# Optimization experiments

Hardware: AMD Instinct MI355X
Metric: run time of the kernel (lower is better)

The kernel has to match this reference:

```python
import jax, jax.numpy as jnp
import numpy as np

N_NODES = 100000
N_EDGES = 640000
D_IN = 128
D_OUT = 128


def setup_inputs() -> dict:
    key = jax.random.key(0)
    k_x, k_w, k_v, k_r, k_c = jax.random.split(key, 5)
    x = jax.random.normal(k_x, (N_NODES, D_IN), dtype=jnp.float32)
    # Xavier-uniform init for weights, zeros for bias (matches module init)
    limit = float(np.sqrt(6.0 / (D_IN + D_OUT)))
    weights = jax.random.uniform(k_w, (D_IN, D_OUT), dtype=jnp.float32,
                                 minval=-limit, maxval=limit)
    bias = jnp.zeros((D_OUT,), dtype=jnp.float32)
    # Sparse normalized adjacency in COO form: value[e] * y[col[e]] scattered to row[e]
    edge_val = jax.random.uniform(k_v, (N_EDGES,), dtype=jnp.float32)
    row = jax.random.randint(k_r, (N_EDGES,), 0, N_NODES, dtype=jnp.int32)
    col = jax.random.randint(k_c, (N_EDGES,), 0, N_NODES, dtype=jnp.int32)
    return {"x": x, "weights": weights, "bias": bias,
            "edge_val": edge_val, "row": row, "col": col}


def reference(x, weights, bias, edge_val, row, col):
    # y = x @ W  (dense GEMM)  [N, D_OUT]
    y = x @ weights
    # SpMM: out[i] = sum_{e: row[e]==i} edge_val[e] * y[col[e]]
    msg = edge_val[:, None] * y[col]            # [E, D_OUT] irregular gather
    agg = jax.ops.segment_sum(msg, row, num_segments=x.shape[0])
    return agg + bias
```

## Files before the change

### kernel.cpp

```cpp
#include <hip/hip_runtime.h>
#include <hip/hip_bf16.h>


#define N_NODES 100000
#define N_EDGES 640000
#define D 128
#define ELL_K 16
#define OVF_CAP 8192
#define NB 391
#define BCAP 2048
#define CHUNK 4096
#define NCHUNKS 157
#define GEMM_BLOCKS 782
#define N_TILES 6250

typedef __attribute__((ext_vector_type(8))) short short8;
typedef __attribute__((ext_vector_type(4))) float f32x4;
typedef __attribute__((ext_vector_type(4))) ushort us4;

__device__ __forceinline__ ushort f2bf(float f) {
    uint u = __float_as_uint(f);
    u += 0x7fff + ((u >> 16) & 1);
    return (ushort)(u >> 16);
}
__device__ __forceinline__ float bflo(uint u) { return __uint_as_float(u << 16); }
__device__ __forceinline__ float bfhi(uint u) { return __uint_as_float(u & 0xffff0000u); }

__global__ __launch_bounds__(256, 2) void gemm_partition(const float* __restrict__ x,
                                                         const float* __restrict__ w,
                                                         ushort* __restrict__ y,
                                                         const float* __restrict__ ev,
                                                         const int* __restrict__ row,
                                                         const int* __restrict__ col,
                                                         int* __restrict__ bucketCnt,
                                                         uint2* __restrict__ es0,
                                                         int* __restrict__ ovfCnt,
                                                         int* __restrict__ ovfRow,
                                                         int* __restrict__ ovfCol,
                                                         float* __restrict__ ovfVal) {
    __shared__ union {
        ushort wt[128 * 128];
        struct { int hist[NB]; int cur[NB]; } p;
    } sm;
    const int tid = threadIdx.x;

    if (blockIdx.x < NCHUNKS) {
        const int base = blockIdx.x * CHUNK;
        for (int t = tid; t < NB; t += 256) sm.p.hist[t] = 0;
        __syncthreads();

        #pragma unroll
        for (int it = 0; it < CHUNK / 256; ++it) {
            int i = base + it * 256 + tid;
            if (i < N_EDGES) atomicAdd(&sm.p.hist[row[i] >> 8], 1);
        }
        __syncthreads();

        for (int t = tid; t < NB; t += 256) {
            int h = sm.p.hist[t];
            int start = (h > 0) ? atomicAdd(&bucketCnt[t], h) : 0;
            sm.p.cur[t] = t * BCAP + start;
        }
        __syncthreads();

        #pragma unroll
        for (int it = 0; it < CHUNK / 256; ++it) {
            int i = base + it * 256 + tid;
            if (i < N_EDGES) {
                int r = row[i];
                int b = r >> 8;
                int p = atomicAdd(&sm.p.cur[b], 1);
                if (p < (b + 1) * BCAP) {
                    uint2 e;
                    e.x = __float_as_uint(ev[i]);
                    e.y = (uint)col[i] | ((uint)(r & 255) << 20);
                    es0[p] = e;
                } else {
                    int q = atomicAdd(ovfCnt, 1);
                    if (q < OVF_CAP) {
                        ovfRow[q] = r;
                        ovfCol[q] = col[i];
                        ovfVal[q] = ev[i];
                    }
                }
            }
        }
        return;
    }

    const int bid = blockIdx.x - NCHUNKS;

    #pragma unroll
    for (int it = 0; it < 16; ++it) {
        int idx4 = tid + it * 256;
        int k = idx4 >> 5;
        int n0 = (idx4 & 31) * 4;
        float4 v = *(const float4*)(w + (size_t)idx4 * 4);
        float vv[4] = {v.x, v.y, v.z, v.w};
        #pragma unroll
        for (int q = 0; q < 4; ++q) {
            int n = n0 + q;
            sm.wt[n * 128 + (k ^ ((n & 7) << 3))] = f2bf(vv[q]);
        }
    }
    __syncthreads();

    const int lane = tid & 63;
    const int l15 = lane & 15;
    const int h = lane >> 4;

    short8 bfr[8][4];
    #pragma unroll
    for (int j = 0; j < 8; ++j) {
        int n = 16 * j + l15;
        #pragma unroll
        for (int ks = 0; ks < 4; ++ks) {
            int k0 = 32 * ks + 8 * h;
            bfr[j][ks] = *(const short8*)&sm.wt[n * 128 + (k0 ^ ((n & 7) << 3))];
        }
    }

    const int t0 = bid * 8 + (tid >> 6) * 2;
    #pragma unroll 1
    for (int rep = 0; rep < 2; ++rep) {
        int t = t0 + rep;
        if (t >= N_TILES) continue;
        const float* xr = x + (size_t)(t * 16 + l15) * D;
        float4 xb[8];
        #pragma unroll
        for (int ks = 0; ks < 4; ++ks) {
            xb[2 * ks]     = *(const float4*)(xr + 32 * ks + 8 * h);
            xb[2 * ks + 1] = *(const float4*)(xr + 32 * ks + 8 * h + 4);
        }
        f32x4 acc[8];
        #pragma unroll
        for (int j = 0; j < 8; ++j) acc[j] = (f32x4){0.f, 0.f, 0.f, 0.f};
        #pragma unroll
        for (int ks = 0; ks < 4; ++ks) {
            const float* p0 = (const float*)&xb[2 * ks];
            const float* p1 = (const float*)&xb[2 * ks + 1];
            short8 a;
            a[0] = f2bf(p0[0]); a[1] = f2bf(p0[1]); a[2] = f2bf(p0[2]); a[3] = f2bf(p0[3]);
            a[4] = f2bf(p1[0]); a[5] = f2bf(p1[1]); a[6] = f2bf(p1[2]); a[7] = f2bf(p1[3]);
            #pragma unroll
            for (int j = 0; j < 8; ++j)
                acc[j] = __builtin_amdgcn_mfma_f32_16x16x32_bf16(bfr[j][ks], a, acc[j], 0, 0, 0);
        }
        ushort* yn = y + (size_t)(t * 16 + l15) * D;
        #pragma unroll
        for (int j = 0; j < 8; ++j) {
            us4 o;
            o.x = f2bf(acc[j][0]); o.y = f2bf(acc[j][1]);
            o.z = f2bf(acc[j][2]); o.w = f2bf(acc[j][3]);
            *(us4*)(yn + 16 * j + 4 * h) = o;
        }
    }
}

__global__ __launch_bounds__(256) void build_ell(const uint2* __restrict__ es0,
                                                 const int* __restrict__ bucketCnt,
                                                 float2* __restrict__ es,
                                                 int* __restrict__ counts,
                                                 int* __restrict__ ovfCnt,
                                                 int* __restrict__ ovfRow,
                                                 int* __restrict__ ovfCol,
                                                 float* __restrict__ ovfVal) {
    __shared__ float2 ell[256 * ELL_K];
    __shared__ int lcnt[256];
    const int tid = threadIdx.x;
    const int b = blockIdx.x;

    lcnt[tid] = 0;
    __syncthreads();

    int cnt = bucketCnt[b];
    if (cnt > BCAP) cnt = BCAP;
    const uint2* src = es0 + (size_t)b * BCAP;

    for (int i = tid; i < cnt; i += 256) {
        uint2 e = src[i];
        int r = e.y >> 20;
        int p = atomicAdd(&lcnt[r], 1);
        if (p < ELL_K) {
            float2 rec;
            rec.x = __uint_as_float(e.x);
            rec.y = __uint_as_float(e.y & 0xFFFFFu);
            ell[r * ELL_K + p] = rec;
        } else {
            int q = atomicAdd(ovfCnt, 1);
            if (q < OVF_CAP) {
                ovfRow[q] = b * 256 + r;
                ovfCol[q] = (int)(e.y & 0xFFFFFu);
                ovfVal[q] = __uint_as_float(e.x);
            }
        }
    }
    __syncthreads();

    const int nbase = b * 256;
    int nvalid = N_NODES - nbase;
    if (nvalid > 256) nvalid = 256;

    if (tid < nvalid) counts[nbase + tid] = lcnt[tid];

    float4* dst4 = (float4*)(es + (size_t)nbase * ELL_K);
    const float4* ell4 = (const float4*)ell;
    for (int t = tid; t < nvalid * (ELL_K / 2); t += 256)
        dst4[t] = ell4[t];
}

__global__ __launch_bounds__(256) void spmm_ell(const ushort* __restrict__ y,
                                                const float2* __restrict__ es,
                                                const int* __restrict__ counts,
                                                const float* __restrict__ bias,
                                                float* __restrict__ out) {
    const int tid = threadIdx.x;
    const int lane = tid & 63;
    const int c16 = lane & 15;
    const int sub = lane >> 4;
    const int wid = blockIdx.x * 4 + (tid >> 6);

    const float4 b0 = *(const float4*)(bias + c16 * 8);
    const float4 b1 = *(const float4*)(bias + c16 * 8 + 4);

    #pragma unroll 1
    for (int rep = 0; rep < 2; ++rep) {
        const int n = wid * 8 + rep * 4 + sub;
        int deg = counts[n];
        if (deg > ELL_K) deg = ELL_K;
        const float4* er = (const float4*)(es + (size_t)n * ELL_K);

        float a0 = 0.f, a1 = 0.f, a2 = 0.f, a3 = 0.f;
        float a4 = 0.f, a5 = 0.f, a6 = 0.f, a7 = 0.f;

        #pragma unroll
        for (int g = 0; g < 4; ++g) {
            if (4 * g < deg) {
                float4 sA = er[2 * g];
                float4 sB = er[2 * g + 1];
                int c0 = __float_as_int(sA.y);
                int c1 = (4 * g + 1 < deg) ? __float_as_int(sA.w) : c0;
                int c2 = (4 * g + 2 < deg) ? __float_as_int(sB.y) : c0;
                int c3 = (4 * g + 3 < deg) ? __float_as_int(sB.w) : c0;
                uint4 u0 = *(const uint4*)(y + ((size_t)c0 << 7) + c16 * 8);
                uint4 u1 = *(const uint4*)(y + ((size_t)c1 << 7) + c16 * 8);
                uint4 u2 = *(const uint4*)(y + ((size_t)c2 << 7) + c16 * 8);
                uint4 u3 = *(const uint4*)(y + ((size_t)c3 << 7) + c16 * 8);
                float v0 = sA.x;
                float v1 = (4 * g + 1 < deg) ? sA.z : 0.f;
                float v2 = (4 * g + 2 < deg) ? sB.x : 0.f;
                float v3 = (4 * g + 3 < deg) ? sB.z : 0.f;
                a0 += v0 * bflo(u0.x); a1 += v0 * bfhi(u0.x);
                a2 += v0 * bflo(u0.y); a3 += v0 * bfhi(u0.y);
                a4 += v0 * bflo(u0.z); a5 += v0 * bfhi(u0.z);
                a6 += v0 * bflo(u0.w); a7 += v0 * bfhi(u0.w);
                a0 += v1 * bflo(u1.x); a1 += v1 * bfhi(u1.x);
                a2 += v1 * bflo(u1.y); a3 += v1 * bfhi(u1.y);
                a4 += v1 * bflo(u1.z); a5 += v1 * bfhi(u1.z);
                a6 += v1 * bflo(u1.w); a7 += v1 * bfhi(u1.w);
                a0 += v2 * bflo(u2.x); a1 += v2 * bfhi(u2.x);
                a2 += v2 * bflo(u2.y); a3 += v2 * bfhi(u2.y);
                a4 += v2 * bflo(u2.z); a5 += v2 * bfhi(u2.z);
                a6 += v2 * bflo(u2.w); a7 += v2 * bfhi(u2.w);
                a0 += v3 * bflo(u3.x); a1 += v3 * bfhi(u3.x);
                a2 += v3 * bflo(u3.y); a3 += v3 * bfhi(u3.y);
                a4 += v3 * bflo(u3.z); a5 += v3 * bfhi(u3.z);
                a6 += v3 * bflo(u3.w); a7 += v3 * bfhi(u3.w);
            }
        }
        float4 o0 = {a0 + b0.x, a1 + b0.y, a2 + b0.z, a3 + b0.w};
        float4 o1 = {a4 + b1.x, a5 + b1.y, a6 + b1.z, a7 + b1.w};
        float* orow = out + ((size_t)n << 7) + c16 * 8;
        *(float4*)orow = o0;
        *(float4*)(orow + 4) = o1;
    }
}

__global__ void ovf_fix(const ushort* __restrict__ y, const int* __restrict__ ovfRow,
                        const int* __restrict__ ovfCol, const float* __restrict__ ovfVal,
                        const int* __restrict__ ovfCnt, float* __restrict__ out) {
    int nOvf = *ovfCnt;
    if (nOvf > OVF_CAP) nOvf = OVF_CAP;
    int total = nOvf * 32;
    for (int idx = blockIdx.x * 256 + threadIdx.x; idx < total; idx += gridDim.x * 256) {
        int e = idx >> 5;
        int c = idx & 31;
        int r = ovfRow[e];
        int col = ovfCol[e];
        float v = ovfVal[e];
        uint2 u = *(const uint2*)(y + ((size_t)col << 7) + c * 4);
        atomicAdd(&out[(size_t)r * D + c * 4 + 0], v * bflo(u.x));
        atomicAdd(&out[(size_t)r * D + c * 4 + 1], v * bfhi(u.x));
        atomicAdd(&out[(size_t)r * D + c * 4 + 2], v * bflo(u.y));
        atomicAdd(&out[(size_t)r * D + c * 4 + 3], v * bfhi(u.y));
    }
}

extern "C" void kernel_launch(void* const* d_in, const int* in_sizes, int n_in,
                              void* d_out, int out_size, void* d_ws, size_t ws_size,
                              hipStream_t stream) {
    const float* x = (const float*)d_in[0];
    const float* w = (const float*)d_in[1];
    const float* bias = (const float*)d_in[2];
    const float* ev = (const float*)d_in[3];
    const int* row = (const int*)d_in[4];
    const int* col = (const int*)d_in[5];
    float* out = (float*)d_out;

    size_t off = 0;
    auto carve = [&](size_t bytes) -> void* {
        void* p = (char*)d_ws + off;
        off += (bytes + 255) & ~(size_t)255;
        return p;
    };
    ushort* y = (ushort*)carve((size_t)N_NODES * D * sizeof(ushort));
    int* counts = (int*)carve((size_t)N_NODES * sizeof(int));
    float2* es = (float2*)carve((size_t)N_NODES * ELL_K * sizeof(float2));
    uint2* es0 = (uint2*)carve((size_t)NB * BCAP * sizeof(uint2));
    int* bucketCnt = (int*)carve((NB + 1) * sizeof(int));
    int* ovfCnt = bucketCnt + NB;
    int* ovfRow = (int*)carve(OVF_CAP * sizeof(int));
    int* ovfCol = (int*)carve(OVF_CAP * sizeof(int));
    float* ovfVal = (float*)carve(OVF_CAP * sizeof(float));

    hipMemsetAsync(bucketCnt, 0, (NB + 1) * sizeof(int), stream);

    gemm_partition<<<NCHUNKS + GEMM_BLOCKS, 256, 0, stream>>>(
        x, w, y, ev, row, col, bucketCnt, es0, ovfCnt, ovfRow, ovfCol, ovfVal);
    build_ell<<<NB, 256, 0, stream>>>(es0, bucketCnt, es, counts,
                                      ovfCnt, ovfRow, ovfCol, ovfVal);
    spmm_ell<<<N_NODES / 32, 256, 0, stream>>>(y, es, counts, bias, out);
    ovf_fix<<<16, 256, 0, stream>>>(y, ovfRow, ovfCol, ovfVal, ovfCnt, out);
}
```

Measured before the change: 86.94 us.

## Split fused GEMM/partition kernel and software-pipeline persistent GEMM waves

Splits the combined GEMM-plus-edge-partition kernel into a persistent GEMM kernel with a grid-stride tile loop that prefetches the next x tile while the current tile's MFMAs run, followed by a separate partition kernel. The bucket counter reset moves from a memset into the GEMM kernel, which removes one launch. The cost is that partitioning no longer runs concurrently with the GEMM, and there is an extra kernel boundary.

```diff
diff --git a/kernel.cpp b/kernel.cpp
--- a/kernel.cpp
+++ b/kernel.cpp
@@ -11,7 +11,6 @@
 #define BCAP 2048
 #define CHUNK 4096
 #define NCHUNKS 157
-#define GEMM_BLOCKS 782
 #define N_TILES 6250
 
 typedef __attribute__((ext_vector_type(8))) short short8;
@@ -26,69 +25,15 @@
 __device__ __forceinline__ float bflo(uint u) { return __uint_as_float(u << 16); }
 __device__ __forceinline__ float bfhi(uint u) { return __uint_as_float(u & 0xffff0000u); }
 
-__global__ __launch_bounds__(256, 2) void gemm_partition(const float* __restrict__ x,
-                                                         const float* __restrict__ w,
-                                                         ushort* __restrict__ y,
-                                                         const float* __restrict__ ev,
-                                                         const int* __restrict__ row,
-                                                         const int* __restrict__ col,
-                                                         int* __restrict__ bucketCnt,
-                                                         uint2* __restrict__ es0,
-                                                         int* __restrict__ ovfCnt,
-                                                         int* __restrict__ ovfRow,
-                                                         int* __restrict__ ovfCol,
-                                                         float* __restrict__ ovfVal) {
-    __shared__ union {
-        ushort wt[128 * 128];
-        struct { int hist[NB]; int cur[NB]; } p;
-    } sm;
+__global__ __launch_bounds__(256, 2) void gemm_xw(const float* __restrict__ x,
+                                                  const float* __restrict__ w,
+                                                  ushort* __restrict__ y,
+                                                  int* __restrict__ bucketCnt) {
+    __shared__ ushort wt[128 * 128];
     const int tid = threadIdx.x;
 
-    if (blockIdx.x < NCHUNKS) {
-        const int base = blockIdx.x * CHUNK;
-        for (int t = tid; t < NB; t += 256) sm.p.hist[t] = 0;
-        __syncthreads();
-
-        #pragma unroll
-        for (int it = 0; it < CHUNK / 256; ++it) {
-            int i = base + it * 256 + tid;
-            if (i < N_EDGES) atomicAdd(&sm.p.hist[row[i] >> 8], 1);
-        }
-        __syncthreads();
-
-        for (int t = tid; t < NB; t += 256) {
-            int h = sm.p.hist[t];
-            int start = (h > 0) ? atomicAdd(&bucketCnt[t], h) : 0;
-            sm.p.cur[t] = t * BCAP + start;
-        }
-        __syncthreads();
-
-        #pragma unroll
-        for (int it = 0; it < CHUNK / 256; ++it) {
-            int i = base + it * 256 + tid;
-            if (i < N_EDGES) {
-                int r = row[i];
-                int b = r >> 8;
-                int p = atomicAdd(&sm.p.cur[b], 1);
-                if (p < (b + 1) * BCAP) {
-                    uint2 e;
-                    e.x = __float_as_uint(ev[i]);
-                    e.y = (uint)col[i] | ((uint)(r & 255) << 20);
-                    es0[p] = e;
-                } else {
-                    int q = atomicAdd(ovfCnt, 1);
-                    if (q < OVF_CAP) {
-                        ovfRow[q] = r;
-                        ovfCol[q] = col[i];
-                        ovfVal[q] = ev[i];
-                    }
-                }
-            }
-        }
-        return;
-    }
-
-    const int bid = blockIdx.x - NCHUNKS;
+    int gz = blockIdx.x * 256 + tid;
+    if (gz <= NB) bucketCnt[gz] = 0;
 
     #pragma unroll
     for (int it = 0; it < 16; ++it) {
@@ -100,7 +45,7 @@
         #pragma unroll
         for (int q = 0; q < 4; ++q) {
             int n = n0 + q;
-            sm.wt[n * 128 + (k ^ ((n & 7) << 3))] = f2bf(vv[q]);
+            wt[n * 128 + (k ^ ((n & 7) << 3))] = f2bf(vv[q]);
         }
     }
     __syncthreads();
@@ -116,43 +61,133 @@
         #pragma unroll
         for (int ks = 0; ks < 4; ++ks) {
             int k0 = 32 * ks + 8 * h;
-            bfr[j][ks] = *(const short8*)&sm.wt[n * 128 + (k0 ^ ((n & 7) << 3))];
-        }
-    }
-
-    const int t0 = bid * 8 + (tid >> 6) * 2;
-    #pragma unroll 1
-    for (int rep = 0; rep < 2; ++rep) {
-        int t = t0 + rep;
-        if (t >= N_TILES) continue;
-        const float* xr = x + (size_t)(t * 16 + l15) * D;
-        float4 xb[8];
-        #pragma unroll
-        for (int ks = 0; ks < 4; ++ks) {
-            xb[2 * ks]     = *(const float4*)(xr + 32 * ks + 8 * h);
-            xb[2 * ks + 1] = *(const float4*)(xr + 32 * ks + 8 * h + 4);
-        }
-        f32x4 acc[8];
-        #pragma unroll
-        for (int j = 0; j < 8; ++j) acc[j] = (f32x4){0.f, 0.f, 0.f, 0.f};
-        #pragma unroll
-        for (int ks = 0; ks < 4; ++ks) {
-            const float* p0 = (const float*)&xb[2 * ks];
-            const float* p1 = (const float*)&xb[2 * ks + 1];
-            short8 a;
-            a[0] = f2bf(p0[0]); a[1] = f2bf(p0[1]); a[2] = f2bf(p0[2]); a[3] = f2bf(p0[3]);
-            a[4] = f2bf(p1[0]); a[5] = f2bf(p1[1]); a[6] = f2bf(p1[2]); a[7] = f2bf(p1[3]);
-            #pragma unroll
-            for (int j = 0; j < 8; ++j)
-                acc[j] = __builtin_amdgcn_mfma_f32_16x16x32_bf16(bfr[j][ks], a, acc[j], 0, 0, 0);
-        }
-        ushort* yn = y + (size_t)(t * 16 + l15) * D;
-        #pragma unroll
-        for (int j = 0; j < 8; ++j) {
-            us4 o;
-            o.x = f2bf(acc[j][0]); o.y = f2bf(acc[j][1]);
-            o.z = f2bf(acc[j][2]); o.w = f2bf(acc[j][3]);
-            *(us4*)(yn + 16 * j + 4 * h) = o;
+            bfr[j][ks] = *(const short8*)&wt[n * 128 + (k0 ^ ((n & 7) << 3))];
+        }
+    }
+
+    const int waveGlobal = blockIdx.x * 4 + (tid >> 6);
+    const int nWaves = gridDim.x * 4;
+
+    int t = waveGlobal;
+    if (t < N_TILES) {
+        short8 a[4];
+        {
+            const float* xr = x + (size_t)(t * 16 + l15) * D;
+            float4 xb[8];
+            #pragma unroll
+            for (int ks = 0; ks < 4; ++ks) {
+                xb[2 * ks]     = *(const float4*)(xr + 32 * ks + 8 * h);
+                xb[2 * ks + 1] = *(const float4*)(xr + 32 * ks + 8 * h + 4);
+            }
+            #pragma unroll
+            for (int ks = 0; ks < 4; ++ks) {
+                const float* p0 = (const float*)&xb[2 * ks];
+                const float* p1 = (const float*)&xb[2 * ks + 1];
+                a[ks][0] = f2bf(p0[0]); a[ks][1] = f2bf(p0[1]);
+                a[ks][2] = f2bf(p0[2]); a[ks][3] = f2bf(p0[3]);
+                a[ks][4] = f2bf(p1[0]); a[ks][5] = f2bf(p1[1]);
+                a[ks][6] = f2bf(p1[2]); a[ks][7] = f2bf(p1[3]);
+            }
+        }
+        #pragma unroll 1
+        while (true) {
+            const int tn = t + nWaves;
+            const bool more = tn < N_TILES;
+
+            float4 xb2[8];
+            if (more) {
+                const float* xr = x + (size_t)(tn * 16 + l15) * D;
+                #pragma unroll
+                for (int ks = 0; ks < 4; ++ks) {
+                    xb2[2 * ks]     = *(const float4*)(xr + 32 * ks + 8 * h);
+                    xb2[2 * ks + 1] = *(const float4*)(xr + 32 * ks + 8 * h + 4);
+                }
+            }
+
+            f32x4 acc[8];
+            #pragma unroll
+            for (int j = 0; j < 8; ++j) acc[j] = (f32x4){0.f, 0.f, 0.f, 0.f};
+            #pragma unroll
+            for (int ks = 0; ks < 4; ++ks) {
+                #pragma unroll
+                for (int j = 0; j < 8; ++j)
+                    acc[j] = __builtin_amdgcn_mfma_f32_16x16x32_bf16(bfr[j][ks], a[ks], acc[j], 0, 0, 0);
+            }
+            ushort* yn = y + (size_t)(t * 16 + l15) * D;
+            #pragma unroll
+            for (int j = 0; j < 8; ++j) {
+                us4 o;
+                o.x = f2bf(acc[j][0]); o.y = f2bf(acc[j][1]);
+                o.z = f2bf(acc[j][2]); o.w = f2bf(acc[j][3]);
+                *(us4*)(yn + 16 * j + 4 * h) = o;
+            }
+
+            if (!more) break;
+            #pragma unroll
+            for (int ks = 0; ks < 4; ++ks) {
+                const float* p0 = (const float*)&xb2[2 * ks];
+                const float* p1 = (const float*)&xb2[2 * ks + 1];
+                a[ks][0] = f2bf(p0[0]); a[ks][1] = f2bf(p0[1]);
+                a[ks][2] = f2bf(p0[2]); a[ks][3] = f2bf(p0[3]);
+                a[ks][4] = f2bf(p1[0]); a[ks][5] = f2bf(p1[1]);
+                a[ks][6] = f2bf(p1[2]); a[ks][7] = f2bf(p1[3]);
+            }
+            t = tn;
+        }
+    }
+}
+
+__global__ __launch_bounds__(256) void partition_edges(const float* __restrict__ ev,
+                                                       const int* __restrict__ row,
+                                                       const int* __restrict__ col,
+                                                       int* __restrict__ bucketCnt,
+                                                       uint2* __restrict__ es0,
+                                                       int* __restrict__ ovfCnt,
+                                                       int* __restrict__ ovfRow,
+                                                       int* __restrict__ ovfCol,
+                                                       float* __restrict__ ovfVal) {
+    __shared__ int hist[NB];
+    __shared__ int cur[NB];
+    const int tid = threadIdx.x;
+    const int base = blockIdx.x * CHUNK;
+
+    for (int t = tid; t < NB; t += 256) hist[t] = 0;
+    __syncthreads();
+
+    #pragma unroll
+    for (int it = 0; it < CHUNK / 256; ++it) {
+        int i = base + it * 256 + tid;
+        if (i < N_EDGES) atomicAdd(&hist[row[i] >> 8], 1);
+    }
+    __syncthreads();
+
+    for (int t = tid; t < NB; t += 256) {
+        int h = hist[t];
+        int start = (h > 0) ? atomicAdd(&bucketCnt[t], h) : 0;
+        cur[t] = t * BCAP + start;
+    }
+    __syncthreads();
+
+    #pragma unroll
+    for (int it = 0; it < CHUNK / 256; ++it) {
+        int i = base + it * 256 + tid;
+        if (i < N_EDGES) {
+            int r = row[i];
+            int b = r >> 8;
+            int p = atomicAdd(&cur[b], 1);
+            if (p < (b + 1) * BCAP) {
+                uint2 e;
+                e.x = __float_as_uint(ev[i]);
+                e.y = (uint)col[i] | ((uint)(r & 255) << 20);
+                es0[p] = e;
+            } else {
+                int q = atomicAdd(ovfCnt, 1);
+                if (q < OVF_CAP) {
+                    ovfRow[q] = r;
+                    ovfCol[q] = col[i];
+                    ovfVal[q] = ev[i];
+                }
+            }
         }
     }
 }
@@ -323,10 +358,9 @@
     int* ovfCol = (int*)carve(OVF_CAP * sizeof(int));
     float* ovfVal = (float*)carve(OVF_CAP * sizeof(float));
 
-    hipMemsetAsync(bucketCnt, 0, (NB + 1) * sizeof(int), stream);
-
-    gemm_partition<<<NCHUNKS + GEMM_BLOCKS, 256, 0, stream>>>(
-        x, w, y, ev, row, col, bucketCnt, es0, ovfCnt, ovfRow, ovfCol, ovfVal);
+    gemm_xw<<<512, 256, 0, stream>>>(x, w, y, bucketCnt);
+    partition_edges<<<NCHUNKS, 256, 0, stream>>>(ev, row, col, bucketCnt, es0,
+                                                 ovfCnt, ovfRow, ovfCol, ovfVal);
     build_ell<<<NB, 256, 0, stream>>>(es0, bucketCnt, es, counts,
                                       ovfCnt, ovfRow, ovfCol, ovfVal);
     spmm_ell<<<N_NODES / 32, 256, 0, stream>>>(y, es, counts, bias, out);
```

Result: no change. 85.89 us (-1.2%).
